# Kernel optimization log

Measured on AMD Instinct MI355X. Metric: run time of the kernel, lower is better.

Reference implementation:

```python
import jax, jax.numpy as jnp
import numpy as np

N = 100000      # nodes
E = 3200000     # edges (avg degree 32)
F_IN = 512
F_OUT = 256


def setup_inputs() -> dict:
    key = jax.random.key(0)
    k1, k2, k3, k4, k5, k6 = jax.random.split(key, 6)
    x = jax.random.normal(k1, (N, F_IN), dtype=jnp.float32)
    row = jax.random.randint(k2, (E,), 0, N)            # destination node of each edge
    col = jax.random.randint(k3, (E,), 0, N)            # source node of each edge
    edge_val = jax.random.uniform(k4, (E,), dtype=jnp.float32)  # normalized adj weights
    stdv = 1.0 / np.sqrt(F_OUT)                         # matches reset_parameters()
    weight = jax.random.uniform(k5, (F_IN, F_OUT), dtype=jnp.float32, minval=-stdv, maxval=stdv)
    bias = jax.random.uniform(k6, (F_OUT,), dtype=jnp.float32, minval=-stdv, maxval=stdv)
    return {"input": x, "weight": weight, "bias": bias, "edge_val": edge_val, "row": row, "col": col}


def reference(input, weight, bias, edge_val, row, col):
    # support = X @ W  (dense projection)
    support = input @ weight                             # [N, F_OUT]
    # SpMM: out[r] += a[r,c] * support[c] over COO edges (torch.spmm(adj, support))
    msgs = edge_val[:, None] * support[col]              # [E, F_OUT] gather + scale
    agg = jax.ops.segment_sum(msgs, row, num_segments=input.shape[0])  # scatter-add
    # np.around(..., decimals=3) applied row-wise in the original
    out = jnp.round(agg * 1000.0) / 1000.0
    return out + bias
```

## Files before the change

kernel.cpp:

```cpp
#include <hip/hip_runtime.h>
#include <hip/hip_bf16.h>

#define N_NODES 100000
#define N_EDGES 3200000
#define FIN 512
#define FOUT 256
#define GEMM_BM 128
#define GEMM_BN 128
#define GEMM_BK 32

#define NP 782
#define CAP_LDS 4608
#define SC_CHUNK 16384

typedef __attribute__((ext_vector_type(8))) short short8;
typedef __attribute__((ext_vector_type(4))) float f32x4;

__device__ __forceinline__ unsigned short f2bf(float f) {
    unsigned u = __float_as_uint(f);
    u += 0x7fffu + ((u >> 16) & 1u);
    return (unsigned short)(u >> 16);
}
__device__ __forceinline__ float bf2f(unsigned short h) {
    return __uint_as_float(((unsigned)h) << 16);
}

__device__ __forceinline__ void gload_lds16(const void* g, void* l) {
    __builtin_amdgcn_global_load_lds(
        (const __attribute__((address_space(1))) unsigned*)g,
        (__attribute__((address_space(3))) unsigned*)l, 16, 0, 0);
}

__global__ __launch_bounds__(256) void prep_weight(const float* __restrict__ W,
                                                   unsigned short* __restrict__ Wt) {
    int idx = blockIdx.x * 256 + threadIdx.x;
    if (idx < FIN * FOUT) {
        int k = idx >> 8;
        int n = idx & 255;
        int s = k >> 5;
        int kk = k & 31;
        int nt = n >> 7;
        int nl = n & 127;
        int kb16 = kk >> 3;
        int u = kb16 ^ (nl & 3) ^ ((nl >> 2) & 3);
        Wt[(size_t)((s * 2 + nt) << 12) + nl * 32 + u * 8 + (kk & 7)] = f2bf(W[idx]);
    }
}

__global__ __launch_bounds__(256)
void gemm_kernel(const float* __restrict__ X, const unsigned short* __restrict__ Wt,
                 unsigned short* __restrict__ support) {
    __shared__ unsigned short A_lds[GEMM_BM][40];
    __shared__ __align__(16) unsigned short bls[4096];

    const int t = threadIdx.x;
    const int lane = t & 63;
    const int w = t >> 6;
    const int wm = w >> 1;
    const int wn = w & 1;
    const int q = lane >> 4;
    const int lr = lane & 15;
    const int m0 = blockIdx.x * GEMM_BM;
    const int nt = blockIdx.y;

    f32x4 acc[4][4];
#pragma unroll
    for (int i = 0; i < 4; i++)
#pragma unroll
        for (int j = 0; j < 4; j++) acc[i][j] = (f32x4)0.0f;

    const int arow = t >> 1;
    const int acol = (t & 1) * 16;
    const bool avalid = (m0 + arow) < N_NODES;
    const float* Xp = X + (size_t)(m0 + arow) * FIN + acol;

    const unsigned short* gB = Wt + ((size_t)nt << 12) + t * 8;
    unsigned short* ldsB0 = &bls[w * 512];
    unsigned short* ldsB1 = &bls[2048 + w * 512];

    for (int s = 0; s < FIN / GEMM_BK; ++s) {
        union { __hip_bfloat162 h[8]; uint4 v[2]; } pk;
        if (avalid) {
            float4 v0 = *(const float4*)(Xp + s * GEMM_BK);
            float4 v1 = *(const float4*)(Xp + s * GEMM_BK + 4);
            float4 v2 = *(const float4*)(Xp + s * GEMM_BK + 8);
            float4 v3 = *(const float4*)(Xp + s * GEMM_BK + 12);
            pk.h[0] = __float22bfloat162_rn(make_float2(v0.x, v0.y));
            pk.h[1] = __float22bfloat162_rn(make_float2(v0.z, v0.w));
            pk.h[2] = __float22bfloat162_rn(make_float2(v1.x, v1.y));
            pk.h[3] = __float22bfloat162_rn(make_float2(v1.z, v1.w));
            pk.h[4] = __float22bfloat162_rn(make_float2(v2.x, v2.y));
            pk.h[5] = __float22bfloat162_rn(make_float2(v2.z, v2.w));
            pk.h[6] = __float22bfloat162_rn(make_float2(v3.x, v3.y));
            pk.h[7] = __float22bfloat162_rn(make_float2(v3.z, v3.w));
        } else {
            pk.v[0] = make_uint4(0, 0, 0, 0);
            pk.v[1] = make_uint4(0, 0, 0, 0);
        }

        __syncthreads();

        gload_lds16(gB + (size_t)s * 8192, ldsB0);
        gload_lds16(gB + (size_t)s * 8192 + 2048, ldsB1);

        *(uint4*)&A_lds[arow][acol] = pk.v[0];
        *(uint4*)&A_lds[arow][acol + 8] = pk.v[1];

        __syncthreads();

        short8 af[4], bfr[4];
#pragma unroll
        for (int i = 0; i < 4; i++) af[i] = *(const short8*)&A_lds[wm * 64 + i * 16 + lr][q * 8];
#pragma unroll
        for (int j = 0; j < 4; j++) {
            int nl = wn * 64 + j * 16 + lr;
            int u = q ^ (nl & 3) ^ ((nl >> 2) & 3);
            bfr[j] = *(const short8*)&bls[nl * 32 + u * 8];
        }
#pragma unroll
        for (int i = 0; i < 4; i++)
#pragma unroll
            for (int j = 0; j < 4; j++)
                acc[i][j] = __builtin_amdgcn_mfma_f32_16x16x32_bf16(af[i], bfr[j], acc[i][j], 0, 0, 0);
    }

    const int n0 = nt * GEMM_BN;
#pragma unroll
    for (int i = 0; i < 4; i++) {
#pragma unroll
        for (int r = 0; r < 4; r++) {
            int gm = m0 + wm * 64 + i * 16 + q * 4 + r;
            if (gm < N_NODES) {
#pragma unroll
                for (int j = 0; j < 4; j++)
                    support[(size_t)gm * FOUT + n0 + wn * 64 + j * 16 + lr] = f2bf(acc[i][j][r]);
            }
        }
    }
}

__global__ __launch_bounds__(256) void part_hist(const int* __restrict__ row,
                                                 unsigned* __restrict__ pcnt) {
    __shared__ unsigned bins[NP];
    for (int i = threadIdx.x; i < NP; i += 256) bins[i] = 0;
    __syncthreads();
    const int e0 = blockIdx.x * 8192;
#pragma unroll
    for (int j = 0; j < 32; ++j) {
        int e = e0 + j * 256 + threadIdx.x;
        if (e < N_EDGES) atomicAdd(&bins[((unsigned)row[e]) >> 7], 1u);
    }
    __syncthreads();
    for (int i = threadIdx.x; i < NP; i += 256)
        if (bins[i]) atomicAdd(&pcnt[i], bins[i]);
}

__global__ __launch_bounds__(1024) void part_scan(const unsigned* __restrict__ pcnt,
                                                  unsigned* __restrict__ base,
                                                  unsigned* __restrict__ cursor,
                                                  unsigned* __restrict__ row_ptr) {
    __shared__ unsigned s[1024];
    const int t = threadIdx.x;
    unsigned v = (t < NP) ? pcnt[t] : 0u;
    s[t] = v;
    __syncthreads();
#pragma unroll
    for (int off = 1; off < 1024; off <<= 1) {
        unsigned tv = (t >= off) ? s[t - off] : 0u;
        __syncthreads();
        s[t] += tv;
        __syncthreads();
    }
    if (t < NP) {
        unsigned b = s[t] - v;
        base[t] = b;
        cursor[t] = b;
    }
    if (t == 0) {
        base[NP] = N_EDGES;
        row_ptr[N_NODES] = N_EDGES;
    }
}

__global__ __launch_bounds__(256) void part_scatter(const int* __restrict__ row,
                                                    const int* __restrict__ col,
                                                    const float* __restrict__ val,
                                                    unsigned* __restrict__ cursor,
                                                    uint2* __restrict__ part) {
    __shared__ unsigned bins[NP];
    __shared__ unsigned gb[NP];
    for (int i = threadIdx.x; i < NP; i += 256) bins[i] = 0;
    __syncthreads();
    const int e0 = blockIdx.x * SC_CHUNK;
#pragma unroll 4
    for (int j = 0; j < SC_CHUNK / 256; ++j) {
        int e = e0 + j * 256 + threadIdx.x;
        if (e < N_EDGES) atomicAdd(&bins[((unsigned)row[e]) >> 7], 1u);
    }
    __syncthreads();
    for (int i = threadIdx.x; i < NP; i += 256) {
        unsigned c = bins[i];
        gb[i] = c ? atomicAdd(&cursor[i], c) : 0u;
        bins[i] = 0;
    }
    __syncthreads();
#pragma unroll 4
    for (int j = 0; j < SC_CHUNK / 256; ++j) {
        int e = e0 + j * 256 + threadIdx.x;
        if (e < N_EDGES) {
            unsigned r = (unsigned)row[e];
            unsigned p = r >> 7;
            unsigned l = atomicAdd(&bins[p], 1u);
            part[gb[p] + l] = make_uint2(((unsigned)col[e]) | ((r & 127u) << 17),
                                         __float_as_uint(val[e]));
        }
    }
}

__global__ __launch_bounds__(256) void part_finalize(const unsigned* __restrict__ base,
                                                     uint2* __restrict__ part,
                                                     unsigned* __restrict__ row_ptr) {
    __shared__ uint2 recs[CAP_LDS];
    __shared__ unsigned ncnt[128], nsc[128], ccur[128];
    const int p = blockIdx.x;
    const int t = threadIdx.x;
    const unsigned b = base[p];
    unsigned cnt = base[p + 1] - b;
    if (cnt > CAP_LDS) cnt = CAP_LDS;
    if (t < 128) ncnt[t] = 0;
    __syncthreads();
    for (unsigned i = t; i < cnt; i += 256) {
        uint2 r = part[b + i];
        recs[i] = r;
        atomicAdd(&ncnt[r.x >> 17], 1u);
    }
    __syncthreads();
    if (t < 128) nsc[t] = ncnt[t];
    __syncthreads();
#pragma unroll
    for (int off = 1; off < 128; off <<= 1) {
        unsigned tv = (t < 128 && t >= off) ? nsc[t - off] : 0u;
        __syncthreads();
        if (t < 128) nsc[t] += tv;
        __syncthreads();
    }
    if (t < 128) {
        unsigned ex = nsc[t] - ncnt[t];
        ccur[t] = ex;
        int node = p * 128 + t;
        if (node < N_NODES) row_ptr[node] = b + ex;
    }
    __syncthreads();
    for (unsigned i = t; i < cnt; i += 256) {
        uint2 r = recs[i];
        unsigned pos = atomicAdd(&ccur[r.x >> 17], 1u);
        part[b + pos] = make_uint2(r.x & 0x1FFFFu, r.y);
    }
}

__global__ __launch_bounds__(256)
void spmm_kernel(const unsigned* __restrict__ row_ptr, const uint2* __restrict__ sorted,
                 const unsigned short* __restrict__ support, const float* __restrict__ bias,
                 float* __restrict__ out) {
    const int lane = threadIdx.x & 63;
    const int n = blockIdx.x * 4 + (threadIdx.x >> 6);
    const unsigned start = __builtin_amdgcn_readfirstlane(row_ptr[n]);
    const unsigned end   = __builtin_amdgcn_readfirstlane(row_ptr[n + 1]);
    const int fo = lane * 4;
    const unsigned short* sp = support + fo;
    float a0 = 0.f, a1 = 0.f, a2 = 0.f, a3 = 0.f;

    unsigned i = start;
    const unsigned nfull = (end - start) >> 4;
    if (nfull) {
        uint2 e[16];
#pragma unroll
        for (int j = 0; j < 16; ++j) e[j] = sorted[i + j];
        for (unsigned bt = 1; bt < nfull; ++bt) {
            ushort4 s[16];
#pragma unroll
            for (int j = 0; j < 16; ++j) s[j] = *(const ushort4*)(sp + (size_t)e[j].x * FOUT);
            uint2 en[16];
#pragma unroll
            for (int j = 0; j < 16; ++j) en[j] = sorted[i + 16 + j];
#pragma unroll
            for (int j = 0; j < 16; ++j) {
                float v = __uint_as_float(e[j].y);
                a0 += v * bf2f(s[j].x); a1 += v * bf2f(s[j].y);
                a2 += v * bf2f(s[j].z); a3 += v * bf2f(s[j].w);
            }
#pragma unroll
            for (int j = 0; j < 16; ++j) e[j] = en[j];
            i += 16;
        }
        ushort4 s[16];
#pragma unroll
        for (int j = 0; j < 16; ++j) s[j] = *(const ushort4*)(sp + (size_t)e[j].x * FOUT);
#pragma unroll
        for (int j = 0; j < 16; ++j) {
            float v = __uint_as_float(e[j].y);
            a0 += v * bf2f(s[j].x); a1 += v * bf2f(s[j].y);
            a2 += v * bf2f(s[j].z); a3 += v * bf2f(s[j].w);
        }
        i += 16;
    }
    if (end - i >= 8) {
        uint2 e[8];
#pragma unroll
        for (int j = 0; j < 8; ++j) e[j] = sorted[i + j];
        ushort4 s[8];
#pragma unroll
        for (int j = 0; j < 8; ++j) s[j] = *(const ushort4*)(sp + (size_t)e[j].x * FOUT);
#pragma unroll
        for (int j = 0; j < 8; ++j) {
            float v = __uint_as_float(e[j].y);
            a0 += v * bf2f(s[j].x); a1 += v * bf2f(s[j].y);
            a2 += v * bf2f(s[j].z); a3 += v * bf2f(s[j].w);
        }
        i += 8;
    }
    for (; i < end; ++i) {
        uint2 e = sorted[i];
        float v = __uint_as_float(e.y);
        ushort4 s0 = *(const ushort4*)(sp + (size_t)e.x * FOUT);
        a0 += v * bf2f(s0.x); a1 += v * bf2f(s0.y); a2 += v * bf2f(s0.z); a3 += v * bf2f(s0.w);
    }

    float4 bv = *(const float4*)(bias + fo);
    float4 r;
    r.x = rintf(a0 * 1000.f) * 0.001f + bv.x;
    r.y = rintf(a1 * 1000.f) * 0.001f + bv.y;
    r.z = rintf(a2 * 1000.f) * 0.001f + bv.z;
    r.w = rintf(a3 * 1000.f) * 0.001f + bv.w;
    *(float4*)(out + (size_t)n * FOUT + fo) = r;
}

extern "C" void kernel_launch(void* const* d_in, const int* in_sizes, int n_in,
                              void* d_out, int out_size, void* d_ws, size_t ws_size,
                              hipStream_t stream) {
    (void)in_sizes; (void)n_in; (void)out_size; (void)ws_size;
    const float* X    = (const float*)d_in[0];
    const float* W    = (const float*)d_in[1];
    const float* bias = (const float*)d_in[2];
    const float* eval = (const float*)d_in[3];
    const int*   row  = (const int*)d_in[4];
    const int*   col  = (const int*)d_in[5];
    float* out = (float*)d_out;

    char* p = (char*)d_ws;
    auto take = [&](size_t bytes) {
        char* r = p;
        p += (bytes + 511) & ~(size_t)511;
        return r;
    };
    unsigned short* support = (unsigned short*)take((size_t)N_NODES * FOUT * 2);
    unsigned short* Wt      = (unsigned short*)take((size_t)FIN * FOUT * 2);
    unsigned*       pcnt    = (unsigned*)take((size_t)NP * 4);
    unsigned*       base    = (unsigned*)take((size_t)(NP + 1) * 4);
    unsigned*       cursor  = (unsigned*)take((size_t)NP * 4);
    unsigned*       row_ptr = (unsigned*)take((size_t)(N_NODES + 1) * 4);
    uint2*          part    = (uint2*)take((size_t)N_EDGES * 8 + 1024);

    hipMemsetAsync(pcnt, 0, (size_t)NP * 4, stream);
    prep_weight<<<(FIN * FOUT) / 256, 256, 0, stream>>>(W, Wt);
    gemm_kernel<<<dim3((N_NODES + GEMM_BM - 1) / GEMM_BM, FOUT / GEMM_BN), 256, 0, stream>>>(X, Wt, support);
    part_hist<<<(N_EDGES + 8191) / 8192, 256, 0, stream>>>(row, pcnt);
    part_scan<<<1, 1024, 0, stream>>>(pcnt, base, cursor, row_ptr);
    part_scatter<<<(N_EDGES + SC_CHUNK - 1) / SC_CHUNK, 256, 0, stream>>>(row, col, eval, cursor, part);
    part_finalize<<<NP, 256, 0, stream>>>(base, part, row_ptr);
    spmm_kernel<<<N_NODES / 4, 256, 0, stream>>>(row_ptr, part, support, bias, out);
}
```

Measured before the change: 760.0 us.

## Use full-width GEMM tiles and split SpMM feature columns across two grid halves

The GEMM now computes all 256 output columns per block with 512 threads (8 waves), so each X tile is read and converted to bf16 once instead of twice across two N-tile blocks. The weight layout is changed to match the wider B tile in LDS. Separately, the SpMM splits the 256 features into two 128-column halves via blockIdx.y, with each lane handling 2 features. This raises parallelism and halves per-wave row width, but the edge list and indices are now read twice.

```diff
diff --git a/kernel.cpp b/kernel.cpp
--- a/kernel.cpp
+++ b/kernel.cpp
@@ -6,7 +6,6 @@
 #define FIN 512
 #define FOUT 256
 #define GEMM_BM 128
-#define GEMM_BN 128
 #define GEMM_BK 32
 
 #define NP 782
@@ -39,29 +38,26 @@
         int n = idx & 255;
         int s = k >> 5;
         int kk = k & 31;
-        int nt = n >> 7;
-        int nl = n & 127;
         int kb16 = kk >> 3;
-        int u = kb16 ^ (nl & 3) ^ ((nl >> 2) & 3);
-        Wt[(size_t)((s * 2 + nt) << 12) + nl * 32 + u * 8 + (kk & 7)] = f2bf(W[idx]);
-    }
-}
-
-__global__ __launch_bounds__(256)
+        int u = kb16 ^ (n & 3) ^ ((n >> 2) & 3);
+        Wt[(size_t)s * 8192 + n * 32 + u * 8 + (kk & 7)] = f2bf(W[idx]);
+    }
+}
+
+__global__ __launch_bounds__(512, 2)
 void gemm_kernel(const float* __restrict__ X, const unsigned short* __restrict__ Wt,
                  unsigned short* __restrict__ support) {
     __shared__ unsigned short A_lds[GEMM_BM][40];
-    __shared__ __align__(16) unsigned short bls[4096];
+    __shared__ __align__(16) unsigned short bls[8192];
 
     const int t = threadIdx.x;
     const int lane = t & 63;
     const int w = t >> 6;
-    const int wm = w >> 1;
-    const int wn = w & 1;
+    const int wm = w >> 2;
+    const int wn = w & 3;
     const int q = lane >> 4;
     const int lr = lane & 15;
     const int m0 = blockIdx.x * GEMM_BM;
-    const int nt = blockIdx.y;
 
     f32x4 acc[4][4];
 #pragma unroll
@@ -69,42 +65,34 @@
 #pragma unroll
         for (int j = 0; j < 4; j++) acc[i][j] = (f32x4)0.0f;
 
-    const int arow = t >> 1;
-    const int acol = (t & 1) * 16;
+    const int arow = t >> 2;
+    const int acol = (t & 3) * 8;
     const bool avalid = (m0 + arow) < N_NODES;
     const float* Xp = X + (size_t)(m0 + arow) * FIN + acol;
 
-    const unsigned short* gB = Wt + ((size_t)nt << 12) + t * 8;
+    const unsigned short* gB = Wt + t * 8;
     unsigned short* ldsB0 = &bls[w * 512];
-    unsigned short* ldsB1 = &bls[2048 + w * 512];
+    unsigned short* ldsB1 = &bls[4096 + w * 512];
 
     for (int s = 0; s < FIN / GEMM_BK; ++s) {
-        union { __hip_bfloat162 h[8]; uint4 v[2]; } pk;
+        union { __hip_bfloat162 h[4]; uint4 v; } pk;
         if (avalid) {
             float4 v0 = *(const float4*)(Xp + s * GEMM_BK);
             float4 v1 = *(const float4*)(Xp + s * GEMM_BK + 4);
-            float4 v2 = *(const float4*)(Xp + s * GEMM_BK + 8);
-            float4 v3 = *(const float4*)(Xp + s * GEMM_BK + 12);
             pk.h[0] = __float22bfloat162_rn(make_float2(v0.x, v0.y));
             pk.h[1] = __float22bfloat162_rn(make_float2(v0.z, v0.w));
             pk.h[2] = __float22bfloat162_rn(make_float2(v1.x, v1.y));
             pk.h[3] = __float22bfloat162_rn(make_float2(v1.z, v1.w));
-            pk.h[4] = __float22bfloat162_rn(make_float2(v2.x, v2.y));
-            pk.h[5] = __float22bfloat162_rn(make_float2(v2.z, v2.w));
-            pk.h[6] = __float22bfloat162_rn(make_float2(v3.x, v3.y));
-            pk.h[7] = __float22bfloat162_rn(make_float2(v3.z, v3.w));
         } else {
-            pk.v[0] = make_uint4(0, 0, 0, 0);
-            pk.v[1] = make_uint4(0, 0, 0, 0);
+            pk.v = make_uint4(0, 0, 0, 0);
         }
 
         __syncthreads();
 
         gload_lds16(gB + (size_t)s * 8192, ldsB0);
-        gload_lds16(gB + (size_t)s * 8192 + 2048, ldsB1);
-
-        *(uint4*)&A_lds[arow][acol] = pk.v[0];
-        *(uint4*)&A_lds[arow][acol + 8] = pk.v[1];
+        gload_lds16(gB + (size_t)s * 8192 + 4096, ldsB1);
+
+        *(uint4*)&A_lds[arow][acol] = pk.v;
 
         __syncthreads();
 
@@ -124,7 +112,6 @@
                 acc[i][j] = __builtin_amdgcn_mfma_f32_16x16x32_bf16(af[i], bfr[j], acc[i][j], 0, 0, 0);
     }
 
-    const int n0 = nt * GEMM_BN;
 #pragma unroll
     for (int i = 0; i < 4; i++) {
 #pragma unroll
@@ -133,7 +120,7 @@
             if (gm < N_NODES) {
 #pragma unroll
                 for (int j = 0; j < 4; j++)
-                    support[(size_t)gm * FOUT + n0 + wn * 64 + j * 16 + lr] = f2bf(acc[i][j][r]);
+                    support[(size_t)gm * FOUT + wn * 64 + j * 16 + lr] = f2bf(acc[i][j][r]);
             }
         }
     }
@@ -266,9 +253,9 @@
     const int n = blockIdx.x * 4 + (threadIdx.x >> 6);
     const unsigned start = __builtin_amdgcn_readfirstlane(row_ptr[n]);
     const unsigned end   = __builtin_amdgcn_readfirstlane(row_ptr[n + 1]);
-    const int fo = lane * 4;
+    const int fo = (blockIdx.y << 7) + lane * 2;
     const unsigned short* sp = support + fo;
-    float a0 = 0.f, a1 = 0.f, a2 = 0.f, a3 = 0.f;
+    float a0 = 0.f, a1 = 0.f;
 
     unsigned i = start;
     const unsigned nfull = (end - start) >> 4;
@@ -277,9 +264,9 @@
 #pragma unroll
         for (int j = 0; j < 16; ++j) e[j] = sorted[i + j];
         for (unsigned bt = 1; bt < nfull; ++bt) {
-            ushort4 s[16];
-#pragma unroll
-            for (int j = 0; j < 16; ++j) s[j] = *(const ushort4*)(sp + (size_t)e[j].x * FOUT);
+            ushort2 s[16];
+#pragma unroll
+            for (int j = 0; j < 16; ++j) s[j] = *(const ushort2*)(sp + (size_t)e[j].x * FOUT);
             uint2 en[16];
 #pragma unroll
             for (int j = 0; j < 16; ++j) en[j] = sorted[i + 16 + j];
@@ -287,20 +274,18 @@
             for (int j = 0; j < 16; ++j) {
                 float v = __uint_as_float(e[j].y);
                 a0 += v * bf2f(s[j].x); a1 += v * bf2f(s[j].y);
-                a2 += v * bf2f(s[j].z); a3 += v * bf2f(s[j].w);
             }
 #pragma unroll
             for (int j = 0; j < 16; ++j) e[j] = en[j];
             i += 16;
         }
-        ushort4 s[16];
-#pragma unroll
-        for (int j = 0; j < 16; ++j) s[j] = *(const ushort4*)(sp + (size_t)e[j].x * FOUT);
+        ushort2 s[16];
+#pragma unroll
+        for (int j = 0; j < 16; ++j) s[j] = *(const ushort2*)(sp + (size_t)e[j].x * FOUT);
 #pragma unroll
         for (int j = 0; j < 16; ++j) {
             float v = __uint_as_float(e[j].y);
             a0 += v * bf2f(s[j].x); a1 += v * bf2f(s[j].y);
-            a2 += v * bf2f(s[j].z); a3 += v * bf2f(s[j].w);
         }
         i += 16;
     }
@@ -308,31 +293,28 @@
         uint2 e[8];
 #pragma unroll
         for (int j = 0; j < 8; ++j) e[j] = sorted[i + j];
-        ushort4 s[8];
-#pragma unroll
-        for (int j = 0; j < 8; ++j) s[j] = *(const ushort4*)(sp + (size_t)e[j].x * FOUT);
+        ushort2 s[8];
+#pragma unroll
+        for (int j = 0; j < 8; ++j) s[j] = *(const ushort2*)(sp + (size_t)e[j].x * FOUT);
 #pragma unroll
         for (int j = 0; j < 8; ++j) {
             float v = __uint_as_float(e[j].y);
             a0 += v * bf2f(s[j].x); a1 += v * bf2f(s[j].y);
-            a2 += v * bf2f(s[j].z); a3 += v * bf2f(s[j].w);
         }
         i += 8;
     }
     for (; i < end; ++i) {
         uint2 e = sorted[i];
         float v = __uint_as_float(e.y);
-        ushort4 s0 = *(const ushort4*)(sp + (size_t)e.x * FOUT);
-        a0 += v * bf2f(s0.x); a1 += v * bf2f(s0.y); a2 += v * bf2f(s0.z); a3 += v * bf2f(s0.w);
-    }
-
-    float4 bv = *(const float4*)(bias + fo);
-    float4 r;
+        ushort2 s0 = *(const ushort2*)(sp + (size_t)e.x * FOUT);
+        a0 += v * bf2f(s0.x); a1 += v * bf2f(s0.y);
+    }
+
+    float2 bv = *(const float2*)(bias + fo);
+    float2 r;
     r.x = rintf(a0 * 1000.f) * 0.001f + bv.x;
     r.y = rintf(a1 * 1000.f) * 0.001f + bv.y;
-    r.z = rintf(a2 * 1000.f) * 0.001f + bv.z;
-    r.w = rintf(a3 * 1000.f) * 0.001f + bv.w;
-    *(float4*)(out + (size_t)n * FOUT + fo) = r;
+    *(float2*)(out + (size_t)n * FOUT + fo) = r;
 }
 
 extern "C" void kernel_launch(void* const* d_in, const int* in_sizes, int n_in,
@@ -363,10 +345,10 @@
 
     hipMemsetAsync(pcnt, 0, (size_t)NP * 4, stream);
     prep_weight<<<(FIN * FOUT) / 256, 256, 0, stream>>>(W, Wt);
-    gemm_kernel<<<dim3((N_NODES + GEMM_BM - 1) / GEMM_BM, FOUT / GEMM_BN), 256, 0, stream>>>(X, Wt, support);
+    gemm_kernel<<<(N_NODES + GEMM_BM - 1) / GEMM_BM, 512, 0, stream>>>(X, Wt, support);
     part_hist<<<(N_EDGES + 8191) / 8192, 256, 0, stream>>>(row, pcnt);
     part_scan<<<1, 1024, 0, stream>>>(pcnt, base, cursor, row_ptr);
     part_scatter<<<(N_EDGES + SC_CHUNK - 1) / SC_CHUNK, 256, 0, stream>>>(row, col, eval, cursor, part);
     part_finalize<<<NP, 256, 0, stream>>>(base, part, row_ptr);
-    spmm_kernel<<<N_NODES / 4, 256, 0, stream>>>(row_ptr, part, support, bias, out);
-}
+    spmm_kernel<<<dim3(N_NODES / 4, 2), 256, 0, stream>>>(row_ptr, part, support, bias, out);
+}
```

After: 705.0 us. 7.2% less time.
